# Optimization experiments

Hardware: AMD Instinct MI355X
Metric: run time of the kernel (lower is better)

Reference implementation:

```python
import jax, jax.numpy as jnp
import numpy as np

CHANNELS = 32


def _mlp(x, W1, b1, W2, b2, W3, b3):
    # FNN: Linear -> ReLU -> Linear -> ReLU -> Linear (last layer linear)
    h = jax.nn.relu(x @ W1 + b1)
    h = jax.nn.relu(h @ W2 + b2)
    return h @ W3 + b3


def setup_inputs() -> dict:
    key = jax.random.key(0)
    ks = jax.random.split(key, 8)
    E = 262144
    C = CHANNELS
    H = 128
    d_in = 4  # 2 * spatial_dim
    d_out = C * (C + 1)  # 1056
    s = lambda fan_in: 1.0 / np.sqrt(fan_in)
    return {
        "pos_i": jax.random.normal(ks[0], (E, 2), jnp.float32),
        "pos_j": jax.random.normal(ks[1], (E, 2), jnp.float32),
        "v_j": jax.random.normal(ks[2], (E, C), jnp.float32),
        "W1": jax.random.normal(ks[3], (d_in, H), jnp.float32) * s(d_in),
        "b1": jnp.zeros((H,), jnp.float32),
        "W2": jax.random.normal(ks[4], (H, H), jnp.float32) * s(H),
        "b2": jnp.zeros((H,), jnp.float32),
        "W3": jax.random.normal(ks[5], (H, d_out), jnp.float32) * s(H),
        "b3": jnp.zeros((d_out,), jnp.float32),
    }


def reference(pos_i, pos_j, v_j, W1, b1, W2, b2, W3, b3):
    C = CHANNELS
    pos_ij = jnp.concatenate((pos_i, pos_j), axis=-1)          # [E, 2*spatial_dim]
    kernel = _mlp(pos_ij, W1, b1, W2, b2, W3, b3)
    kernel = kernel.reshape(-1, C, C + 1)                      # [E, C, C+1]
    mat, bias = kernel[..., :, :-1], kernel[..., :, -1]        # [E,C,C], [E,C]
    return jnp.einsum('eij,ej->ei', mat, v_j) + bias           # [E, C]
```

## Files before the change

kernel.cpp:

```cpp
#include <hip/hip_runtime.h>


#define E_TOTAL 262144
#define EPB 256
#define NBLK (E_TOTAL / EPB)
#define NEED_WS (524288ull + 67108864ull)

typedef float f32x4 __attribute__((ext_vector_type(4)));
typedef short s8v  __attribute__((ext_vector_type(8)));
typedef short s4v  __attribute__((ext_vector_type(4)));
typedef unsigned int u32;

__device__ __forceinline__ unsigned short f2bf(float x) {
  unsigned u = __float_as_uint(x);
  u += 0x7fffu + ((u >> 16) & 1u);
  return (unsigned short)(u >> 16);
}

__device__ __forceinline__ void ld16_g2l(const void* g, void* l) {
  __builtin_amdgcn_global_load_lds((const __attribute__((address_space(1))) u32*)g,
                                   (__attribute__((address_space(3))) u32*)l, 16, 0, 0);
}

__global__ void prep_pack(const float* __restrict__ W2, const float* __restrict__ W3,
                          const float* __restrict__ b3,
                          unsigned short* __restrict__ Wg2, unsigned short* __restrict__ W2f,
                          unsigned short* __restrict__ b3f, float* __restrict__ b3c) {
  int idx = blockIdx.x * 256 + threadIdx.x;
  if (idx < 135168) {
    int k = idx / 1056, c = idx % 1056;
    int i = c / 33, jc = c % 33;
    int col = jc * 32 + i;
    int nnt = col >> 4, low = col & 15;
    int nn = (nnt & 1) ? (33 + (nnt >> 1)) : (nnt >> 1);
    int ks = k >> 5, kr = k & 31;
    int lane = ((kr >> 3) << 4) + low;
    int jj = k & 7;
    Wg2[((nn * 4 + ks) * 64 + lane) * 8 + jj] = f2bf(W3[idx]);
  }
  if (idx < 16384) {
    int k = idx >> 7, n = idx & 127;
    int ks = k >> 5, kr = k & 31;
    int nt = n >> 4, low = n & 15;
    int l = ((kr >> 3) << 4) + low;
    int jj = k & 7;
    W2f[((ks * 8 + nt) * 64 + l) * 8 + jj] = f2bf(W2[idx]);
  }
  if (idx < 1024) {
    int jj = idx & 7, lane = (idx >> 3) & 63, ih = idx >> 9;
    int j = ((lane >> 4) << 3) + jj, i = ih * 16 + (lane & 15);
    b3f[idx] = f2bf(b3[i * 33 + j]);
  }
  if (idx < 32) b3c[idx] = b3[idx * 33 + 32];
}

__global__ __launch_bounds__(256, 3) void h2_pass(
    const float* __restrict__ pos_i, const float* __restrict__ pos_j,
    const float* __restrict__ W1, const float* __restrict__ b1,
    const float* __restrict__ b2, const unsigned short* __restrict__ W2f,
    unsigned short* __restrict__ h2frag) {
  __shared__ __attribute__((aligned(16))) char smem[34816];
  unsigned short* h1c = (unsigned short*)smem;
  unsigned short* h2n = (unsigned short*)(smem + 17408);

  const int tid = threadIdx.x;
  const int w = tid >> 6, lane = tid & 63, q = lane >> 4, ln = lane & 15;
  const int B0h = blockIdx.x * 64;

  const int hh0 = (tid & 31) * 4;
  float w1r[4][4], b1r4[4], b2r[8];
#pragma unroll
  for (int d = 0; d < 4; ++d)
#pragma unroll
    for (int u = 0; u < 4; ++u) w1r[d][u] = W1[d * 128 + hh0 + u];
#pragma unroll
  for (int u = 0; u < 4; ++u) b1r4[u] = b1[hh0 + u];
#pragma unroll
  for (int s = 0; s < 8; ++s) b2r[s] = b2[s * 16 + ln];

#pragma unroll
  for (int half = 0; half < 8; ++half) {
    int ee = (tid >> 5) + half * 8;
    int eg = B0h + ee;
    float2 pi = *(const float2*)(pos_i + (size_t)eg * 2);
    float2 pj = *(const float2*)(pos_j + (size_t)eg * 2);
    s4v hv;
#pragma unroll
    for (int u = 0; u < 4; ++u) {
      float o = b1r4[u] + pi.x * w1r[0][u] + pi.y * w1r[1][u] +
                pj.x * w1r[2][u] + pj.y * w1r[3][u];
      hv[u] = (short)f2bf(fmaxf(o, 0.f));
    }
    *(s4v*)&h1c[ee * 136 + hh0] = hv;
  }
  __syncthreads();

#pragma unroll
  for (int s = 0; s < 8; ++s) {
    f32x4 a4 = {0.f, 0.f, 0.f, 0.f};
#pragma unroll
    for (int ks = 0; ks < 4; ++ks) {
      s8v afr = *(const s8v*)&h1c[(w * 16 + ln) * 136 + ks * 32 + q * 8];
      s8v bfr = *(const s8v*)(W2f + ((ks * 8 + s) * 64 + lane) * 8);
      a4 = __builtin_amdgcn_mfma_f32_16x16x32_bf16(afr, bfr, a4, 0, 0, 0);
    }
    int eb = w * 16 + q * 4;
    int kc = s * 16 + ln;
#pragma unroll
    for (int r = 0; r < 4; ++r)
      h2n[(eb + r) * 136 + kc] = f2bf(fmaxf(a4[r] + b2r[s], 0.f));
  }
  __syncthreads();

  {
    int f = tid >> 4, g = f >> 2, ks = f & 3, s = tid & 15;
    unsigned short* dst = h2frag + ((size_t)(blockIdx.x * 16 + f)) * 512;
#pragma unroll
    for (int r4 = 0; r4 < 4; ++r4) {
      int l = s * 4 + r4;
      s8v v = *(const s8v*)&h2n[(g * 16 + (l & 15)) * 136 + ks * 32 + (l >> 4) * 8];
      *(s8v*)&dst[l * 8] = v;
    }
  }
}

__device__ __forceinline__ void tile_load(s8v (&dst)[4], const unsigned short* __restrict__ Wg2,
                                          int n, int lane) {
  const s8v* src = (const s8v*)(Wg2 + (size_t)n * 2048 + lane * 8);
#pragma unroll
  for (int ks = 0; ks < 4; ++ks) dst[ks] = src[ks * 64];
}

template <int IH>
__device__ __forceinline__ void tile_compute(const s8v (&bf)[4], const float* __restrict__ vt,
                                             int j, int eoff,
                                             const s8v (&af)[4][4], float (&oa)[2][4][4]) {
  const f32x4 zero4 = {0.f, 0.f, 0.f, 0.f};
  const float* vp = vt + j * 260 + eoff;
#pragma unroll
  for (int m = 0; m < 4; ++m) {
    f32x4 p = __builtin_amdgcn_mfma_f32_16x16x32_bf16(af[m][0], bf[0], zero4, 0, 0, 0);
#pragma unroll
    for (int ks = 1; ks < 4; ++ks)
      p = __builtin_amdgcn_mfma_f32_16x16x32_bf16(af[m][ks], bf[ks], p, 0, 0, 0);
    f32x4 vv = *(const f32x4*)(vp + m * 16);
#pragma unroll
    for (int r = 0; r < 4; ++r) oa[IH][m][r] += vv[r] * p[r];
  }
}

__global__ __launch_bounds__(256, 2) void g_pass(
    const float* __restrict__ vj, const unsigned short* __restrict__ Wg2,
    const unsigned short* __restrict__ b3f, const float* __restrict__ b3c,
    const unsigned short* __restrict__ h2frag, float* __restrict__ out) {
  __shared__ __attribute__((aligned(16))) char smem[34320];
  float* vt = (float*)smem;

  const int tid = threadIdx.x;
  const int w = tid >> 6, lane = tid & 63, q = lane >> 4, ln = lane & 15;
  const int B0 = blockIdx.x * EPB;
  const int eoff = w * 64 + q * 4;

  s8v af[4][4];
#pragma unroll
  for (int m = 0; m < 4; ++m)
#pragma unroll
    for (int ks = 0; ks < 4; ++ks)
      af[m][ks] = *(const s8v*)&h2frag[((size_t)(blockIdx.x * 16 + w * 4 + m) * 4 + ks) * 512 + lane * 8];

  float oa[2][4][4];
  {
    s8v av[4];
#pragma unroll
    for (int m = 0; m < 4; ++m) {
      int e = B0 + w * 64 + m * 16 + ln;
      const float4 va = *(const float4*)(vj + (size_t)e * 32 + q * 8);
      const float4 vb = *(const float4*)(vj + (size_t)e * 32 + q * 8 + 4);
      s8v t;
      t[0] = (short)f2bf(va.x); t[1] = (short)f2bf(va.y);
      t[2] = (short)f2bf(va.z); t[3] = (short)f2bf(va.w);
      t[4] = (short)f2bf(vb.x); t[5] = (short)f2bf(vb.y);
      t[6] = (short)f2bf(vb.z); t[7] = (short)f2bf(vb.w);
      av[m] = t;
    }
#pragma unroll
    for (int ih = 0; ih < 2; ++ih) {
      s8v b3fr = *(const s8v*)(b3f + (ih * 64 + lane) * 8);
      float cbv = b3c[ih * 16 + ln];
      f32x4 ci = {cbv, cbv, cbv, cbv};
#pragma unroll
      for (int m = 0; m < 4; ++m) {
        f32x4 p = __builtin_amdgcn_mfma_f32_16x16x32_bf16(av[m], b3fr, ci, 0, 0, 0);
#pragma unroll
        for (int r = 0; r < 4; ++r) oa[ih][m][r] = p[r];
      }
    }
  }

  s8v bf[4];
  tile_load(bf, Wg2, 0, lane);

  {
    const float* vrow = vj + (size_t)(B0 + tid) * 32;
#pragma unroll
    for (int j4 = 0; j4 < 8; ++j4) {
      float4 vv = *(const float4*)(vrow + j4 * 4);
      vt[(j4 * 4 + 0) * 260 + tid] = vv.x;
      vt[(j4 * 4 + 1) * 260 + tid] = vv.y;
      vt[(j4 * 4 + 2) * 260 + tid] = vv.z;
      vt[(j4 * 4 + 3) * 260 + tid] = vv.w;
    }
    vt[32 * 260 + tid] = 1.0f;
  }

#pragma unroll 1
  for (int n = 0; n < 33; ++n) {
    tile_compute<0>(bf, vt, n, eoff, af, oa);
    tile_load(bf, Wg2, n + 1, lane);
  }
#pragma unroll 1
  for (int n = 33; n < 66; ++n) {
    tile_compute<1>(bf, vt, n - 33, eoff, af, oa);
    tile_load(bf, Wg2, n + 1, lane);
  }

#pragma unroll
  for (int m = 0; m < 4; ++m)
#pragma unroll
    for (int ih = 0; ih < 2; ++ih)
#pragma unroll
      for (int r = 0; r < 4; ++r) {
        int e = B0 + w * 64 + m * 16 + q * 4 + r;
        out[(size_t)e * 32 + ih * 16 + ln] = oa[ih][m][r];
      }
}

__global__ __launch_bounds__(256, 2) void fnn_fused(
    const float* __restrict__ pos_i, const float* __restrict__ pos_j,
    const float* __restrict__ vj, const float* __restrict__ W1,
    const float* __restrict__ b1, const float* __restrict__ b2,
    const unsigned short* __restrict__ W2f, const unsigned short* __restrict__ Wg2,
    const unsigned short* __restrict__ b3f, const float* __restrict__ b3c,
    float* __restrict__ out) {
  __shared__ __attribute__((aligned(16))) char smem[67584];
  float* vt = (float*)smem;
  unsigned short* h1c = (unsigned short*)smem;
  unsigned short* h2n = (unsigned short*)(smem + 17408);
  unsigned short* W2L = (unsigned short*)(smem + 34816);

  const int tid = threadIdx.x;
  const int w = tid >> 6, lane = tid & 63, q = lane >> 4, ln = lane & 15;
  const int B0 = blockIdx.x * EPB;
  const int eoff = w * 64 + q * 4;

  {
    const unsigned short* src = W2f + tid * 8;
    char* dstb = smem + 34816 + w * 1024;
#pragma unroll
    for (int cc = 0; cc < 8; ++cc)
      ld16_g2l(src + cc * 2048, dstb + cc * 4096);
  }

  float oa[2][4][4];
  {
    s8v av[4];
#pragma unroll
    for (int m = 0; m < 4; ++m) {
      int e = B0 + w * 64 + m * 16 + ln;
      const float4 va = *(const float4*)(vj + (size_t)e * 32 + q * 8);
      const float4 vb = *(const float4*)(vj + (size_t)e * 32 + q * 8 + 4);
      s8v t;
      t[0] = (short)f2bf(va.x); t[1] = (short)f2bf(va.y);
      t[2] = (short)f2bf(va.z); t[3] = (short)f2bf(va.w);
      t[4] = (short)f2bf(vb.x); t[5] = (short)f2bf(vb.y);
      t[6] = (short)f2bf(vb.z); t[7] = (short)f2bf(vb.w);
      av[m] = t;
    }
#pragma unroll
    for (int ih = 0; ih < 2; ++ih) {
      s8v b3fr = *(const s8v*)(b3f + (ih * 64 + lane) * 8);
      float cbv = b3c[ih * 16 + ln];
      f32x4 ci = {cbv, cbv, cbv, cbv};
#pragma unroll
      for (int m = 0; m < 4; ++m) {
        f32x4 p = __builtin_amdgcn_mfma_f32_16x16x32_bf16(av[m], b3fr, ci, 0, 0, 0);
#pragma unroll
        for (int r = 0; r < 4; ++r) oa[ih][m][r] = p[r];
      }
    }
  }

  const int hh0 = (tid & 15) * 8;
  float w1r[4][8], b1r[8], b2r[8];
#pragma unroll
  for (int d = 0; d < 4; ++d)
#pragma unroll
    for (int u = 0; u < 8; ++u) w1r[d][u] = W1[d * 128 + hh0 + u];
#pragma unroll
  for (int u = 0; u < 8; ++u) b1r[u] = b1[hh0 + u];
#pragma unroll
  for (int s = 0; s < 8; ++s) b2r[s] = b2[s * 16 + ln];

  s8v af[4][4];
  for (int qtr = 0; qtr < 4; ++qtr) {
#pragma unroll
    for (int half = 0; half < 4; ++half) {
      int ee = (tid >> 4) + half * 16;
      int eg = B0 + qtr * 64 + ee;
      float2 pi = *(const float2*)(pos_i + (size_t)eg * 2);
      float2 pj = *(const float2*)(pos_j + (size_t)eg * 2);
      s8v hv;
#pragma unroll
      for (int u = 0; u < 8; ++u) {
        float o = b1r[u] + pi.x * w1r[0][u] + pi.y * w1r[1][u] +
                  pj.x * w1r[2][u] + pj.y * w1r[3][u];
        hv[u] = (short)f2bf(fmaxf(o, 0.f));
      }
      *(s8v*)&h1c[ee * 136 + hh0] = hv;
    }
    __syncthreads();
#pragma unroll
    for (int s = 0; s < 8; ++s) {
      f32x4 a4 = {0.f, 0.f, 0.f, 0.f};
#pragma unroll
      for (int ks = 0; ks < 4; ++ks) {
        s8v afr = *(const s8v*)&h1c[(w * 16 + ln) * 136 + ks * 32 + q * 8];
        s8v bfr = *(const s8v*)&W2L[((ks * 8 + s) * 64 + lane) * 8];
        a4 = __builtin_amdgcn_mfma_f32_16x16x32_bf16(afr, bfr, a4, 0, 0, 0);
      }
      int eb = w * 16 + q * 4;
      int kc = s * 16 + ln;
#pragma unroll
      for (int r = 0; r < 4; ++r)
        h2n[(eb + r) * 136 + kc] = f2bf(fmaxf(a4[r] + b2r[s], 0.f));
    }
    __syncthreads();
    if (w == qtr) {
#pragma unroll
      for (int m = 0; m < 4; ++m)
#pragma unroll
        for (int ks = 0; ks < 4; ++ks)
          af[m][ks] = *(const s8v*)&h2n[(m * 16 + ln) * 136 + ks * 32 + q * 8];
    }
    __syncthreads();
  }

  s8v bf[4];
  tile_load(bf, Wg2, 0, lane);

  {
    const float* vrow = vj + (size_t)(B0 + tid) * 32;
#pragma unroll
    for (int j4 = 0; j4 < 8; ++j4) {
      float4 vv = *(const float4*)(vrow + j4 * 4);
      vt[(j4 * 4 + 0) * 260 + tid] = vv.x;
      vt[(j4 * 4 + 1) * 260 + tid] = vv.y;
      vt[(j4 * 4 + 2) * 260 + tid] = vv.z;
      vt[(j4 * 4 + 3) * 260 + tid] = vv.w;
    }
    vt[32 * 260 + tid] = 1.0f;
  }

#pragma unroll 1
  for (int n = 0; n < 33; ++n) {
    tile_compute<0>(bf, vt, n, eoff, af, oa);
    tile_load(bf, Wg2, n + 1, lane);
  }
#pragma unroll 1
  for (int n = 33; n < 66; ++n) {
    tile_compute<1>(bf, vt, n - 33, eoff, af, oa);
    tile_load(bf, Wg2, n + 1, lane);
  }

#pragma unroll
  for (int m = 0; m < 4; ++m)
#pragma unroll
    for (int ih = 0; ih < 2; ++ih)
#pragma unroll
      for (int r = 0; r < 4; ++r) {
        int e = B0 + w * 64 + m * 16 + q * 4 + r;
        out[(size_t)e * 32 + ih * 16 + ln] = oa[ih][m][r];
      }
}

extern "C" void kernel_launch(void* const* d_in, const int* in_sizes, int n_in,
                              void* d_out, int out_size, void* d_ws, size_t ws_size,
                              hipStream_t stream) {
  const float* pos_i = (const float*)d_in[0];
  const float* pos_j = (const float*)d_in[1];
  const float* vj    = (const float*)d_in[2];
  const float* W1    = (const float*)d_in[3];
  const float* b1    = (const float*)d_in[4];
  const float* W2    = (const float*)d_in[5];
  const float* b2    = (const float*)d_in[6];
  const float* W3    = (const float*)d_in[7];
  const float* b3    = (const float*)d_in[8];
  float* outp = (float*)d_out;

  unsigned short* Wg2 = (unsigned short*)d_ws;
  unsigned short* W2f = (unsigned short*)((char*)d_ws + 270336);
  unsigned short* b3f = (unsigned short*)((char*)d_ws + 303104);
  float*          b3c = (float*)((char*)d_ws + 305152);
  unsigned short* h2frag = (unsigned short*)((char*)d_ws + 524288);

  prep_pack<<<528, 256, 0, stream>>>(W2, W3, b3, Wg2, W2f, b3f, b3c);
  if (ws_size >= NEED_WS) {
    h2_pass<<<E_TOTAL / 64, 256, 0, stream>>>(pos_i, pos_j, W1, b1, b2, W2f, h2frag);
    g_pass<<<NBLK, 256, 0, stream>>>(vj, Wg2, b3f, b3c, h2frag, outp);
  } else {
    fnn_fused<<<NBLK, 256, 0, stream>>>(pos_i, pos_j, vj, W1, b1, b2, W2f, Wg2, b3f, b3c, outp);
  }
}
```

Measured before the change: 202.5 us.

## Stage W2 in LDS for h2 pass and split g_pass accumulators per half

h2_pass now processes 256 edges per block in four 64-edge quarters. W2 is staged once into shared memory via global_load_lds instead of being read from global memory for every MFMA, and each thread computes 8 hidden units per edge instead of 4. g_pass keeps only one half of the output accumulators live at a time: it initializes, accumulates and stores each 16-channel half separately. That cuts register pressure, so launch bounds are raised to 3 blocks per CU. The costs are that vj is re-read for the second bias init and h2_pass uses more LDS per block.

```diff
diff --git a/kernel.cpp b/kernel.cpp
--- a/kernel.cpp
+++ b/kernel.cpp
@@ -8,7 +8,6 @@
 
 typedef float f32x4 __attribute__((ext_vector_type(4)));
 typedef short s8v  __attribute__((ext_vector_type(8)));
-typedef short s4v  __attribute__((ext_vector_type(4)));
 typedef unsigned int u32;
 
 __device__ __forceinline__ unsigned short f2bf(float x) {
@@ -59,67 +58,79 @@
     const float* __restrict__ W1, const float* __restrict__ b1,
     const float* __restrict__ b2, const unsigned short* __restrict__ W2f,
     unsigned short* __restrict__ h2frag) {
-  __shared__ __attribute__((aligned(16))) char smem[34816];
+  __shared__ __attribute__((aligned(16))) char smem[67584];
   unsigned short* h1c = (unsigned short*)smem;
   unsigned short* h2n = (unsigned short*)(smem + 17408);
+  unsigned short* W2L = (unsigned short*)(smem + 34816);
 
   const int tid = threadIdx.x;
   const int w = tid >> 6, lane = tid & 63, q = lane >> 4, ln = lane & 15;
-  const int B0h = blockIdx.x * 64;
-
-  const int hh0 = (tid & 31) * 4;
-  float w1r[4][4], b1r4[4], b2r[8];
+  const int B0 = blockIdx.x * EPB;
+
+  {
+    const unsigned short* src = W2f + tid * 8;
+    char* dstb = smem + 34816 + w * 1024;
+#pragma unroll
+    for (int cc = 0; cc < 8; ++cc)
+      ld16_g2l(src + cc * 2048, dstb + cc * 4096);
+  }
+
+  const int hh0 = (tid & 15) * 8;
+  float w1r[4][8], b1r[8], b2r[8];
 #pragma unroll
   for (int d = 0; d < 4; ++d)
 #pragma unroll
-    for (int u = 0; u < 4; ++u) w1r[d][u] = W1[d * 128 + hh0 + u];
-#pragma unroll
-  for (int u = 0; u < 4; ++u) b1r4[u] = b1[hh0 + u];
+    for (int u = 0; u < 8; ++u) w1r[d][u] = W1[d * 128 + hh0 + u];
+#pragma unroll
+  for (int u = 0; u < 8; ++u) b1r[u] = b1[hh0 + u];
 #pragma unroll
   for (int s = 0; s < 8; ++s) b2r[s] = b2[s * 16 + ln];
 
-#pragma unroll
-  for (int half = 0; half < 8; ++half) {
-    int ee = (tid >> 5) + half * 8;
-    int eg = B0h + ee;
-    float2 pi = *(const float2*)(pos_i + (size_t)eg * 2);
-    float2 pj = *(const float2*)(pos_j + (size_t)eg * 2);
-    s4v hv;
-#pragma unroll
-    for (int u = 0; u < 4; ++u) {
-      float o = b1r4[u] + pi.x * w1r[0][u] + pi.y * w1r[1][u] +
-                pj.x * w1r[2][u] + pj.y * w1r[3][u];
-      hv[u] = (short)f2bf(fmaxf(o, 0.f));
-    }
-    *(s4v*)&h1c[ee * 136 + hh0] = hv;
-  }
-  __syncthreads();
-
-#pragma unroll
-  for (int s = 0; s < 8; ++s) {
-    f32x4 a4 = {0.f, 0.f, 0.f, 0.f};
-#pragma unroll
-    for (int ks = 0; ks < 4; ++ks) {
-      s8v afr = *(const s8v*)&h1c[(w * 16 + ln) * 136 + ks * 32 + q * 8];
-      s8v bfr = *(const s8v*)(W2f + ((ks * 8 + s) * 64 + lane) * 8);
-      a4 = __builtin_amdgcn_mfma_f32_16x16x32_bf16(afr, bfr, a4, 0, 0, 0);
-    }
-    int eb = w * 16 + q * 4;
-    int kc = s * 16 + ln;
-#pragma unroll
-    for (int r = 0; r < 4; ++r)
-      h2n[(eb + r) * 136 + kc] = f2bf(fmaxf(a4[r] + b2r[s], 0.f));
-  }
-  __syncthreads();
-
-  {
-    int f = tid >> 4, g = f >> 2, ks = f & 3, s = tid & 15;
-    unsigned short* dst = h2frag + ((size_t)(blockIdx.x * 16 + f)) * 512;
-#pragma unroll
-    for (int r4 = 0; r4 < 4; ++r4) {
-      int l = s * 4 + r4;
-      s8v v = *(const s8v*)&h2n[(g * 16 + (l & 15)) * 136 + ks * 32 + (l >> 4) * 8];
-      *(s8v*)&dst[l * 8] = v;
+  for (int qtr = 0; qtr < 4; ++qtr) {
+#pragma unroll
+    for (int half = 0; half < 4; ++half) {
+      int ee = (tid >> 4) + half * 16;
+      int eg = B0 + qtr * 64 + ee;
+      float2 pi = *(const float2*)(pos_i + (size_t)eg * 2);
+      float2 pj = *(const float2*)(pos_j + (size_t)eg * 2);
+      s8v hv;
+#pragma unroll
+      for (int u = 0; u < 8; ++u) {
+        float o = b1r[u] + pi.x * w1r[0][u] + pi.y * w1r[1][u] +
+                  pj.x * w1r[2][u] + pj.y * w1r[3][u];
+        hv[u] = (short)f2bf(fmaxf(o, 0.f));
+      }
+      *(s8v*)&h1c[ee * 136 + hh0] = hv;
+    }
+    __syncthreads();
+
+#pragma unroll
+    for (int s = 0; s < 8; ++s) {
+      f32x4 a4 = {0.f, 0.f, 0.f, 0.f};
+#pragma unroll
+      for (int ks = 0; ks < 4; ++ks) {
+        s8v afr = *(const s8v*)&h1c[(w * 16 + ln) * 136 + ks * 32 + q * 8];
+        s8v bfr = *(const s8v*)&W2L[((ks * 8 + s) * 64 + lane) * 8];
+        a4 = __builtin_amdgcn_mfma_f32_16x16x32_bf16(afr, bfr, a4, 0, 0, 0);
+      }
+      int eb = w * 16 + q * 4;
+      int kc = s * 16 + ln;
+#pragma unroll
+      for (int r = 0; r < 4; ++r)
+        h2n[(eb + r) * 136 + kc] = f2bf(fmaxf(a4[r] + b2r[s], 0.f));
+    }
+    __syncthreads();
+
+    {
+      int f = tid >> 4, g = f >> 2, ks = f & 3, s = tid & 15;
+      unsigned short* dst =
+          h2frag + ((size_t)(blockIdx.x * 16 + qtr * 4 + g) * 4 + ks) * 512;
+#pragma unroll
+      for (int r4 = 0; r4 < 4; ++r4) {
+        int l = s * 4 + r4;
+        s8v v = *(const s8v*)&h2n[(g * 16 + (l & 15)) * 136 + ks * 32 + (l >> 4) * 8];
+        *(s8v*)&dst[l * 8] = v;
+      }
     }
   }
 }
@@ -131,25 +142,58 @@
   for (int ks = 0; ks < 4; ++ks) dst[ks] = src[ks * 64];
 }
 
-template <int IH>
 __device__ __forceinline__ void tile_compute(const s8v (&bf)[4], const float* __restrict__ vt,
                                              int j, int eoff,
-                                             const s8v (&af)[4][4], float (&oa)[2][4][4]) {
+                                             const s8v (&af)[4][4], float (&oa)[4][4]) {
   const f32x4 zero4 = {0.f, 0.f, 0.f, 0.f};
   const float* vp = vt + j * 260 + eoff;
 #pragma unroll
   for (int m = 0; m < 4; ++m) {
+    f32x4 vv = *(const f32x4*)(vp + m * 16);
     f32x4 p = __builtin_amdgcn_mfma_f32_16x16x32_bf16(af[m][0], bf[0], zero4, 0, 0, 0);
 #pragma unroll
     for (int ks = 1; ks < 4; ++ks)
       p = __builtin_amdgcn_mfma_f32_16x16x32_bf16(af[m][ks], bf[ks], p, 0, 0, 0);
-    f32x4 vv = *(const f32x4*)(vp + m * 16);
-#pragma unroll
-    for (int r = 0; r < 4; ++r) oa[IH][m][r] += vv[r] * p[r];
-  }
-}
-
-__global__ __launch_bounds__(256, 2) void g_pass(
+#pragma unroll
+    for (int r = 0; r < 4; ++r) oa[m][r] += vv[r] * p[r];
+  }
+}
+
+__device__ __forceinline__ void init_oa(float (&oa)[4][4], const float* __restrict__ vj,
+                                        const unsigned short* __restrict__ b3f,
+                                        const float* __restrict__ b3c,
+                                        int B0, int w, int q, int ln, int lane, int ih) {
+  s8v b3fr = *(const s8v*)(b3f + (ih * 64 + lane) * 8);
+  float cbv = b3c[ih * 16 + ln];
+  f32x4 ci = {cbv, cbv, cbv, cbv};
+#pragma unroll
+  for (int m = 0; m < 4; ++m) {
+    int e = B0 + w * 64 + m * 16 + ln;
+    const float4 va = *(const float4*)(vj + (size_t)e * 32 + q * 8);
+    const float4 vb = *(const float4*)(vj + (size_t)e * 32 + q * 8 + 4);
+    s8v t;
+    t[0] = (short)f2bf(va.x); t[1] = (short)f2bf(va.y);
+    t[2] = (short)f2bf(va.z); t[3] = (short)f2bf(va.w);
+    t[4] = (short)f2bf(vb.x); t[5] = (short)f2bf(vb.y);
+    t[6] = (short)f2bf(vb.z); t[7] = (short)f2bf(vb.w);
+    f32x4 p = __builtin_amdgcn_mfma_f32_16x16x32_bf16(t, b3fr, ci, 0, 0, 0);
+#pragma unroll
+    for (int r = 0; r < 4; ++r) oa[m][r] = p[r];
+  }
+}
+
+__device__ __forceinline__ void store_half(float* __restrict__ out, const float (&oa)[4][4],
+                                           int B0, int w, int q, int ln, int ih) {
+#pragma unroll
+  for (int m = 0; m < 4; ++m)
+#pragma unroll
+    for (int r = 0; r < 4; ++r) {
+      int e = B0 + w * 64 + m * 16 + q * 4 + r;
+      out[(size_t)e * 32 + ih * 16 + ln] = oa[m][r];
+    }
+}
+
+__global__ __launch_bounds__(256, 3) void g_pass(
     const float* __restrict__ vj, const unsigned short* __restrict__ Wg2,
     const unsigned short* __restrict__ b3f, const float* __restrict__ b3c,
     const unsigned short* __restrict__ h2frag, float* __restrict__ out) {
@@ -167,35 +211,6 @@
 #pragma unroll
     for (int ks = 0; ks < 4; ++ks)
       af[m][ks] = *(const s8v*)&h2frag[((size_t)(blockIdx.x * 16 + w * 4 + m) * 4 + ks) * 512 + lane * 8];
-
-  float oa[2][4][4];
-  {
-    s8v av[4];
-#pragma unroll
-    for (int m = 0; m < 4; ++m) {
-      int e = B0 + w * 64 + m * 16 + ln;
-      const float4 va = *(const float4*)(vj + (size_t)e * 32 + q * 8);
-      const float4 vb = *(const float4*)(vj + (size_t)e * 32 + q * 8 + 4);
-      s8v t;
-      t[0] = (short)f2bf(va.x); t[1] = (short)f2bf(va.y);
-      t[2] = (short)f2bf(va.z); t[3] = (short)f2bf(va.w);
-      t[4] = (short)f2bf(vb.x); t[5] = (short)f2bf(vb.y);
-      t[6] = (short)f2bf(vb.z); t[7] = (short)f2bf(vb.w);
-      av[m] = t;
-    }
-#pragma unroll
-    for (int ih = 0; ih < 2; ++ih) {
-      s8v b3fr = *(const s8v*)(b3f + (ih * 64 + lane) * 8);
-      float cbv = b3c[ih * 16 + ln];
-      f32x4 ci = {cbv, cbv, cbv, cbv};
-#pragma unroll
-      for (int m = 0; m < 4; ++m) {
-        f32x4 p = __builtin_amdgcn_mfma_f32_16x16x32_bf16(av[m], b3fr, ci, 0, 0, 0);
-#pragma unroll
-        for (int r = 0; r < 4; ++r) oa[ih][m][r] = p[r];
-      }
-    }
-  }
 
   s8v bf[4];
   tile_load(bf, Wg2, 0, lane);
@@ -213,26 +228,42 @@
     vt[32 * 260 + tid] = 1.0f;
   }
 
+  float oa[4][4];
+  init_oa(oa, vj, b3f, b3c, B0, w, q, ln, lane, 0);
+
 #pragma unroll 1
   for (int n = 0; n < 33; ++n) {
-    tile_compute<0>(bf, vt, n, eoff, af, oa);
+    tile_compute(bf, vt, n, eoff, af, oa);
     tile_load(bf, Wg2, n + 1, lane);
   }
+
+  store_half(out, oa, B0, w, q, ln, 0);
+  init_oa(oa, vj, b3f, b3c, B0, w, q, ln, lane, 1);
+
 #pragma unroll 1
   for (int n = 33; n < 66; ++n) {
-    tile_compute<1>(bf, vt, n - 33, eoff, af, oa);
+    tile_compute(bf, vt, n - 33, eoff, af, oa);
     tile_load(bf, Wg2, n + 1, lane);
   }
-
-#pragma unroll
-  for (int m = 0; m < 4; ++m)
-#pragma unroll
-    for (int ih = 0; ih < 2; ++ih)
-#pragma unroll
-      for (int r = 0; r < 4; ++r) {
-        int e = B0 + w * 64 + m * 16 + q * 4 + r;
-        out[(size_t)e * 32 + ih * 16 + ln] = oa[ih][m][r];
-      }
+  store_half(out, oa, B0, w, q, ln, 1);
+}
+
+template <int IH>
+__device__ __forceinline__ void tile_compute2(const s8v (&bf)[4], const float* __restrict__ vt,
+                                              int j, int eoff,
+                                              const s8v (&af)[4][4], float (&oa)[2][4][4]) {
+  const f32x4 zero4 = {0.f, 0.f, 0.f, 0.f};
+  const float* vp = vt + j * 260 + eoff;
+#pragma unroll
+  for (int m = 0; m < 4; ++m) {
+    f32x4 p = __builtin_amdgcn_mfma_f32_16x16x32_bf16(af[m][0], bf[0], zero4, 0, 0, 0);
+#pragma unroll
+    for (int ks = 1; ks < 4; ++ks)
+      p = __builtin_amdgcn_mfma_f32_16x16x32_bf16(af[m][ks], bf[ks], p, 0, 0, 0);
+    f32x4 vv = *(const f32x4*)(vp + m * 16);
+#pragma unroll
+    for (int r = 0; r < 4; ++r) oa[IH][m][r] += vv[r] * p[r];
+  }
 }
 
 __global__ __launch_bounds__(256, 2) void fnn_fused(
@@ -363,12 +394,12 @@
 
 #pragma unroll 1
   for (int n = 0; n < 33; ++n) {
-    tile_compute<0>(bf, vt, n, eoff, af, oa);
+    tile_compute2<0>(bf, vt, n, eoff, af, oa);
     tile_load(bf, Wg2, n + 1, lane);
   }
 #pragma unroll 1
   for (int n = 33; n < 66; ++n) {
-    tile_compute<1>(bf, vt, n - 33, eoff, af, oa);
+    tile_compute2<1>(bf, vt, n - 33, eoff, af, oa);
     tile_load(bf, Wg2, n + 1, lane);
   }
 
@@ -405,7 +436,7 @@
 
   prep_pack<<<528, 256, 0, stream>>>(W2, W3, b3, Wg2, W2f, b3f, b3c);
   if (ws_size >= NEED_WS) {
-    h2_pass<<<E_TOTAL / 64, 256, 0, stream>>>(pos_i, pos_j, W1, b1, b2, W2f, h2frag);
+    h2_pass<<<NBLK, 256, 0, stream>>>(pos_i, pos_j, W1, b1, b2, W2f, h2frag);
     g_pass<<<NBLK, 256, 0, stream>>>(vj, Wg2, b3f, b3c, h2frag, outp);
   } else {
     fnn_fused<<<NBLK, 256, 0, stream>>>(pos_i, pos_j, vj, W1, b1, b2, W2f, Wg2, b3f, b3c, outp);
```

Measured after the change: 191.8 us. -5.3%, faster.
